# Performance work log

Hardware: AMD Instinct MI355X
Metric: run time of the kernel (lower is better)

## Reference

```python
import jax, jax.numpy as jnp
import numpy as np

B, S, D = 1, 4096, 768
H = 12
HD = D // H  # 64


def setup_inputs() -> dict:
    key = jax.random.key(0)
    ks = jax.random.split(key, 6)
    sc = 1.0 / np.sqrt(D)
    return {
        "x": jax.random.normal(ks[0], (B, S, D), dtype=jnp.float32),
        "wq": jax.random.normal(ks[1], (D, D), dtype=jnp.float32) * sc,
        "wk": jax.random.normal(ks[2], (D, D), dtype=jnp.float32) * sc,
        "wv": jax.random.normal(ks[3], (D, D), dtype=jnp.float32) * sc,
        "wo": jax.random.normal(ks[4], (D, D), dtype=jnp.float32) * sc,
        "bo": jax.random.normal(ks[5], (D,), dtype=jnp.float32) * 0.02,
    }


def reference(x, wq, wk, wv, wo, bo):
    b, n, _ = x.shape
    # projections (torch Linear: x @ W.T; here weights stored as (d_in, d_out))
    q = (x @ wq).reshape(b, n, H, HD).transpose(0, 2, 1, 3)  # b h n d
    k = (x @ wk).reshape(b, n, H, HD).transpose(0, 2, 1, 3)
    v = (x @ wv).reshape(b, n, H, HD).transpose(0, 2, 1, 3)
    scores = jnp.einsum("bhqd,bhkd->bhqk", q, k)
    causal = jnp.tril(jnp.ones((n, n), dtype=bool))  # True = keep
    scores = jnp.where(causal, scores, -jnp.inf)
    weights = jax.nn.softmax(scores / np.sqrt(HD), axis=-1)
    ctx = jnp.einsum("bhqk,bhkd->bhqd", weights, v)
    ctx = ctx.transpose(0, 2, 1, 3).reshape(b, n, D)
    return ctx @ wo + bo
```

## Files before the change

kernel.cpp:

```cpp
#include <hip/hip_runtime.h>


typedef short bf16x8 __attribute__((ext_vector_type(8)));
typedef float f32x4 __attribute__((ext_vector_type(4)));
typedef unsigned short u16;

static constexpr int S_LEN = 4096;
static constexpr int DIM   = 768;
static constexpr int NH    = 12;
static constexpr float QSCALE = 0.125f * 1.44269504088896340736f;

__device__ inline u16 f2bf(float f) {
  union { float f; unsigned int u; } v; v.f = f;
  unsigned int r = v.u + 0x7FFFu + ((v.u >> 16) & 1u);
  return (u16)(r >> 16);
}

__device__ inline void gload_lds16(const u16* g, u16* s) {
  __builtin_amdgcn_global_load_lds(
      (const __attribute__((address_space(1))) unsigned int*)g,
      (__attribute__((address_space(3))) unsigned int*)s, 16, 0, 0);
}

__global__ __launch_bounds__(256)
void prep_kernel(const float* __restrict__ x, const float* __restrict__ w0,
                 const float* __restrict__ w1, const float* __restrict__ w2,
                 const float* __restrict__ w3, u16* __restrict__ xb,
                 u16* __restrict__ t0, u16* __restrict__ t1,
                 u16* __restrict__ t2, u16* __restrict__ t3) {
  if (blockIdx.z == 4) {
    const size_t n = (size_t)S_LEN * DIM;
    const int id = blockIdx.y * 12 + blockIdx.x;
    const size_t stride = (size_t)144 * 256 * 8;
    for (size_t i = ((size_t)id * 256 + threadIdx.x) * 8; i < n; i += stride) {
      const float4 a = *(const float4*)(x + i);
      const float4 b = *(const float4*)(x + i + 4);
      bf16x8 o;
      o[0] = (short)f2bf(a.x); o[1] = (short)f2bf(a.y);
      o[2] = (short)f2bf(a.z); o[3] = (short)f2bf(a.w);
      o[4] = (short)f2bf(b.x); o[5] = (short)f2bf(b.y);
      o[6] = (short)f2bf(b.z); o[7] = (short)f2bf(b.w);
      *(bf16x8*)(xb + i) = o;
    }
    return;
  }
  __shared__ float T[64][65];
  const float* src; u16* dst;
  switch (blockIdx.z) {
    case 0: src = w0; dst = t0; break;
    case 1: src = w1; dst = t1; break;
    case 2: src = w2; dst = t2; break;
    default: src = w3; dst = t3; break;
  }
  const int k0 = blockIdx.y * 64, n0 = blockIdx.x * 64;
  const int r = threadIdx.x >> 2, c0 = (threadIdx.x & 3) * 16;
#pragma unroll
  for (int i = 0; i < 4; ++i) {
    const float4 v = *(const float4*)(src + (size_t)(k0 + r) * DIM + n0 + c0 + i * 4);
    T[r][c0 + i * 4 + 0] = v.x;
    T[r][c0 + i * 4 + 1] = v.y;
    T[r][c0 + i * 4 + 2] = v.z;
    T[r][c0 + i * 4 + 3] = v.w;
  }
  __syncthreads();
  bf16x8 o0, o1;
#pragma unroll
  for (int i = 0; i < 8; ++i) {
    o0[i] = (short)f2bf(T[c0 + i][r]);
    o1[i] = (short)f2bf(T[c0 + 8 + i][r]);
  }
  *(bf16x8*)(dst + (size_t)(n0 + r) * DIM + k0 + c0) = o0;
  *(bf16x8*)(dst + (size_t)(n0 + r) * DIM + k0 + c0 + 8) = o1;
}

template <int MODE>
__global__ __launch_bounds__(256)
void mfma_gemm_kernel(const u16* __restrict__ A, const u16* __restrict__ Bq,
                      const u16* __restrict__ Bk, const u16* __restrict__ Bv,
                      const float* __restrict__ bias, u16* __restrict__ Qb,
                      u16* __restrict__ Kb, u16* __restrict__ VT,
                      float* __restrict__ Out) {
  constexpr int MT = (MODE == 0) ? 4 : 2;
  constexpr int BM = MT * 32;
  __shared__ __align__(16) u16 Al[BM * 64];
  __shared__ __align__(16) u16 Bl[96 * 64];

  const int tid  = threadIdx.x;
  const int wv   = tid >> 6;
  const int lane = tid & 63;
  const int quad = lane >> 4;
  const int l16  = lane & 15;
  const int wr = wv >> 1, wc = wv & 1;
  const int m0 = blockIdx.y * BM;
  const int n0 = blockIdx.x * 96;

  int wi = 0, nb = n0;
  const u16* BT = Bq;
  if (MODE == 0) {
    wi = n0 / DIM;
    nb = n0 - wi * DIM;
    BT = (wi == 0) ? Bq : (wi == 1) ? Bk : Bv;
  }

  const int sr8 = lane >> 3;
  const int sc  = ((lane & 7) ^ sr8) * 8;
  const int key = (l16 & 7);

  f32x4 acc[MT][3] = {};

  for (int k0 = 0; k0 < DIM; k0 += 64) {
    __syncthreads();
#pragma unroll
    for (int j = 0; j < MT; ++j)
      gload_lds16(A + (size_t)(m0 + wv * (BM / 4) + j * 8 + sr8) * DIM + k0 + sc,
                  &Al[(wv * (BM / 4) + j * 8) * 64]);
#pragma unroll
    for (int j = 0; j < 3; ++j)
      gload_lds16(BT + (size_t)(nb + wv * 24 + j * 8 + sr8) * DIM + k0 + sc,
                  &Bl[(wv * 24 + j * 8) * 64]);
    __syncthreads();

#pragma unroll
    for (int kh = 0; kh < 2; ++kh) {
      const int cb = kh * 4;
      bf16x8 af[MT], bfr[3];
#pragma unroll
      for (int mt = 0; mt < MT; ++mt) {
        const int row = wr * (BM / 2) + mt * 16 + l16;
        af[mt] = *(const bf16x8*)&Al[row * 64 + ((cb + quad) ^ key) * 8];
      }
#pragma unroll
      for (int nt = 0; nt < 3; ++nt) {
        const int row = wc * 48 + nt * 16 + l16;
        bfr[nt] = *(const bf16x8*)&Bl[row * 64 + ((cb + quad) ^ key) * 8];
      }
#pragma unroll
      for (int mt = 0; mt < MT; ++mt)
#pragma unroll
        for (int nt = 0; nt < 3; ++nt)
          acc[mt][nt] = __builtin_amdgcn_mfma_f32_16x16x32_bf16(
              af[mt], bfr[nt], acc[mt][nt], 0, 0, 0);
    }
  }

  const float sc_out = (MODE == 0 && wi == 0) ? QSCALE : 1.0f;
#pragma unroll
  for (int mt = 0; mt < MT; ++mt) {
#pragma unroll
    for (int nt = 0; nt < 3; ++nt) {
      const int row = m0 + wr * (BM / 2) + mt * 16 + quad * 4;
      const int nc  = wc * 48 + nt * 16 + l16;
      if (MODE == 0) {
        const int ncol = nb + nc;
        if (wi < 2) {
          u16* dst = (wi == 0) ? Qb : Kb;
#pragma unroll
          for (int r = 0; r < 4; ++r)
            dst[(size_t)(row + r) * DIM + ncol] = f2bf(acc[mt][nt][r] * sc_out);
        } else {
          u16 pk[4];
#pragma unroll
          for (int r = 0; r < 4; ++r) pk[r] = f2bf(acc[mt][nt][r]);
          unsigned long long v;
          __builtin_memcpy(&v, pk, 8);
          *(unsigned long long*)(VT + (size_t)ncol * S_LEN + row) = v;
        }
      } else {
        const int ncol = n0 + nc;
        const float bvv = bias[ncol];
#pragma unroll
        for (int r = 0; r < 4; ++r)
          Out[(size_t)(row + r) * DIM + ncol] = acc[mt][nt][r] + bvv;
      }
    }
  }
}

__global__ __launch_bounds__(256)
void attn_mfma_kernel(const u16* __restrict__ Qb, const u16* __restrict__ Kb,
                      const u16* __restrict__ VTb, u16* __restrict__ ctx) {
  __shared__ __align__(16) u16 Ql[32 * 72];
  __shared__ __align__(16) u16 Kl[128 * 64];
  __shared__ __align__(16) u16 Vl[64 * 128];
  __shared__ __align__(16) u16 Pl[4][16 * 72];
  __shared__ float lbuf[256];

  const int tid  = threadIdx.x;
  const int w    = tid >> 6;
  const int lane = tid & 63;
  const int quad = lane >> 4;
  const int l16  = lane & 15;
  const int qw   = w >> 1;
  const int kw   = w & 1;
  const int key  = l16 & 7;

  const int id = blockIdx.x;
  const int rc = id & 7, slot = id >> 3;
  const int h  = (slot < 64) ? rc : 8 + (rc >> 1);
  const int bx = (slot < 64) ? slot : ((rc & 1) * 32 + (slot - 64));

  const int sr8  = lane >> 3;
  const int scK  = ((lane & 7) ^ sr8) * 8;
  const int sr16 = lane >> 4;

  bf16x8 ones;
#pragma unroll
  for (int i = 0; i < 8; ++i) ones[i] = (short)0x3F80;

#pragma unroll 1
  for (int side = 0; side < 2; ++side) {
    const int qt = side ? (127 - bx) : bx;
    const int q0 = qt * 32;

    __syncthreads();
    {
      const int row = tid >> 3, col = (tid & 7) * 8;
      *(bf16x8*)&Ql[row * 72 + col] =
          *(const bf16x8*)(Qb + (size_t)(q0 + row) * DIM + h * 64 + col);
    }

    f32x4 o[4] = {};
    f32x4 l_acc = {};

    const int nkt = qt / 2 + 1;
    const int niter = (nkt + 1) >> 1;
    const int my_last = nkt - 1;

#pragma unroll 1
    for (int i = 0; i < niter; ++i) {
      const int k0g = i * 128;
      __syncthreads();
#pragma unroll
      for (int j = 0; j < 4; ++j)
        gload_lds16(Kb + (size_t)(k0g + w * 32 + j * 8 + sr8) * DIM + h * 64 + scK,
                    &Kl[(w * 32 + j * 8) * 64]);
#pragma unroll
      for (int j = 0; j < 4; ++j) {
        const int vrow = w * 16 + j * 4 + sr16;
        const int vcol = ((lane & 15) ^ (vrow & 7)) * 8;
        gload_lds16(VTb + (size_t)(h * 64 + vrow) * S_LEN + k0g + vcol,
                    &Vl[(w * 16 + j * 4) * 128]);
      }
      __syncthreads();

      const int kt_w = 2 * i + kw;
      if (kt_w < nkt) {
        const bf16x8 aq0 = *(const bf16x8*)&Ql[(qw * 16 + l16) * 72 + quad * 8];
        const bf16x8 aq1 = *(const bf16x8*)&Ql[(qw * 16 + l16) * 72 + 32 + quad * 8];
        f32x4 s[4];
#pragma unroll
        for (int t = 0; t < 4; ++t) {
          const int row = kw * 64 + t * 16 + l16;
          const bf16x8 bk0 = *(const bf16x8*)&Kl[row * 64 + (quad ^ key) * 8];
          const bf16x8 bk1 = *(const bf16x8*)&Kl[row * 64 + ((quad ^ 4) ^ key) * 8];
          s[t] = __builtin_amdgcn_mfma_f32_16x16x32_bf16(aq0, bk0, f32x4{0.f,0.f,0.f,0.f}, 0, 0, 0);
          s[t] = __builtin_amdgcn_mfma_f32_16x16x32_bf16(aq1, bk1, s[t], 0, 0, 0);
        }

        if (kt_w == my_last) {
#pragma unroll
          for (int t = 0; t < 4; ++t)
#pragma unroll
            for (int r = 0; r < 4; ++r) {
              const int kvg = k0g + kw * 64 + t * 16 + l16;
              const int qg  = q0 + qw * 16 + quad * 4 + r;
              float p = __builtin_amdgcn_exp2f(s[t][r]);
              if (kvg > qg) p = 0.f;
              Pl[w][(quad * 4 + r) * 72 + t * 16 + l16] =
                  (u16)((__float_as_uint(p) + 0x8000u) >> 16);
            }
        } else {
#pragma unroll
          for (int t = 0; t < 4; ++t)
#pragma unroll
            for (int r = 0; r < 4; ++r) {
              const float p = __builtin_amdgcn_exp2f(s[t][r]);
              Pl[w][(quad * 4 + r) * 72 + t * 16 + l16] =
                  (u16)((__float_as_uint(p) + 0x8000u) >> 16);
            }
        }

        const bf16x8 pa0 = *(const bf16x8*)&Pl[w][l16 * 72 + quad * 8];
        const bf16x8 pa1 = *(const bf16x8*)&Pl[w][l16 * 72 + 32 + quad * 8];
#pragma unroll
        for (int t = 0; t < 4; ++t) {
          const int row = t * 16 + l16;
          const int c0 = (kw * 8 + quad) ^ key;
          const int c1 = (kw * 8 + quad + 4) ^ key;
          const bf16x8 vb0 = *(const bf16x8*)&Vl[row * 128 + c0 * 8];
          const bf16x8 vb1 = *(const bf16x8*)&Vl[row * 128 + c1 * 8];
          o[t] = __builtin_amdgcn_mfma_f32_16x16x32_bf16(vb0, pa0, o[t], 0, 0, 0);
          o[t] = __builtin_amdgcn_mfma_f32_16x16x32_bf16(vb1, pa1, o[t], 0, 0, 0);
        }
        l_acc = __builtin_amdgcn_mfma_f32_16x16x32_bf16(ones, pa0, l_acc, 0, 0, 0);
        l_acc = __builtin_amdgcn_mfma_f32_16x16x32_bf16(ones, pa1, l_acc, 0, 0, 0);
      }
    }

    __syncthreads();
    f32x4* Obuf = (f32x4*)Kl;
    const int ga = (kw == 0) ? 2 : 0;
    const int keep = 2 - ga;
    Obuf[(w * 2 + 0) * 64 + lane] = o[ga + 0];
    Obuf[(w * 2 + 1) * 64 + lane] = o[ga + 1];
    lbuf[w * 64 + lane] = l_acc[0];
    __syncthreads();
    o[keep + 0] += Obuf[((w ^ 1) * 2 + 0) * 64 + lane];
    o[keep + 1] += Obuf[((w ^ 1) * 2 + 1) * 64 + lane];
    const float l = l_acc[0] + lbuf[(w ^ 1) * 64 + lane];
    const float inv = 1.f / l;

    const int qrow = q0 + qw * 16 + l16;
#pragma unroll
    for (int s = 0; s < 2; ++s) {
      const int t = keep + s;
      u16 pk[4];
#pragma unroll
      for (int r = 0; r < 4; ++r) pk[r] = f2bf(o[t][r] * inv);
      unsigned long long v;
      __builtin_memcpy(&v, pk, 8);
      *(unsigned long long*)(ctx + (size_t)qrow * DIM + h * 64 + t * 16 + quad * 4) = v;
    }
  }
}

extern "C" void kernel_launch(void* const* d_in, const int* in_sizes, int n_in,
                              void* d_out, int out_size, void* d_ws,
                              size_t ws_size, hipStream_t stream) {
  const float* x  = (const float*)d_in[0];
  const float* wq = (const float*)d_in[1];
  const float* wk = (const float*)d_in[2];
  const float* wv = (const float*)d_in[3];
  const float* wo = (const float*)d_in[4];
  const float* bo = (const float*)d_in[5];

  const size_t n_x = (size_t)S_LEN * DIM;
  const size_t n_w = (size_t)DIM * DIM;
  u16* xb  = (u16*)d_ws;
  u16* wtq = xb + n_x;
  u16* wtk = wtq + n_w;
  u16* wtv = wtk + n_w;
  u16* wto = wtv + n_w;
  u16* Qb  = wto + n_w;
  u16* Kb  = Qb + n_x;
  u16* VTb = Kb + n_x;
  u16* ctx = VTb + n_x;

  prep_kernel<<<dim3(12, 12, 5), 256, 0, stream>>>(
      x, wq, wk, wv, wo, xb, wtq, wtk, wtv, wto);

  mfma_gemm_kernel<0><<<dim3(24, 32), 256, 0, stream>>>(
      xb, wtq, wtk, wtv, nullptr, Qb, Kb, VTb, nullptr);

  attn_mfma_kernel<<<dim3(768), 256, 0, stream>>>(Qb, Kb, VTb, ctx);

  mfma_gemm_kernel<1><<<dim3(8, 64), 256, 0, stream>>>(
      ctx, wto, nullptr, nullptr, bo, nullptr, nullptr, nullptr, (float*)d_out);
}
```

Baseline: 191.3 us.

## Load K/V/Q fragments directly from global memory instead of staging through LDS

The attention kernel stops staging Q, K and V^T tiles in shared memory with global_load_lds and block-wide barriers. Each wave now loads its own MFMA operand fragments straight from global memory into registers and walks its key tiles independently. The per-iteration __syncthreads are gone and LDS usage shrinks, which may allow higher occupancy. The cost is that the two query waves sharing a key tile now each fetch it separately, so the loads are redundant and less coalesced, and the extra register pressure and exposed global latency may outweigh the removed barriers.

After: 300.0 us. 56.9% more time.

```diff
diff --git a/kernel.cpp b/kernel.cpp
--- a/kernel.cpp
+++ b/kernel.cpp
@@ -179,11 +179,9 @@
 __global__ __launch_bounds__(256)
 void attn_mfma_kernel(const u16* __restrict__ Qb, const u16* __restrict__ Kb,
                       const u16* __restrict__ VTb, u16* __restrict__ ctx) {
-  __shared__ __align__(16) u16 Ql[32 * 72];
-  __shared__ __align__(16) u16 Kl[128 * 64];
-  __shared__ __align__(16) u16 Vl[64 * 128];
   __shared__ __align__(16) u16 Pl[4][16 * 72];
-  __shared__ float lbuf[256];
+  __shared__ __align__(16) f32x4 Obuf[8][64];
+  __shared__ float lbuf[4][64];
 
   const int tid  = threadIdx.x;
   const int w    = tid >> 6;
@@ -192,17 +190,12 @@
   const int l16  = lane & 15;
   const int qw   = w >> 1;
   const int kw   = w & 1;
-  const int key  = l16 & 7;
 
   const int id = blockIdx.x;
   const int rc = id & 7, slot = id >> 3;
   const int h  = (slot < 64) ? rc : 8 + (rc >> 1);
   const int bx = (slot < 64) ? slot : ((rc & 1) * 32 + (slot - 64));
 
-  const int sr8  = lane >> 3;
-  const int scK  = ((lane & 7) ^ sr8) * 8;
-  const int sr16 = lane >> 4;
-
   bf16x8 ones;
 #pragma unroll
   for (int i = 0; i < 8; ++i) ones[i] = (short)0x3F80;
@@ -212,102 +205,81 @@
     const int qt = side ? (127 - bx) : bx;
     const int q0 = qt * 32;
 
-    __syncthreads();
-    {
-      const int row = tid >> 3, col = (tid & 7) * 8;
-      *(bf16x8*)&Ql[row * 72 + col] =
-          *(const bf16x8*)(Qb + (size_t)(q0 + row) * DIM + h * 64 + col);
-    }
+    const u16* qptr = Qb + (size_t)(q0 + qw * 16 + l16) * DIM + h * 64 + quad * 8;
+    const bf16x8 aq0 = *(const bf16x8*)(qptr);
+    const bf16x8 aq1 = *(const bf16x8*)(qptr + 32);
 
     f32x4 o[4] = {};
     f32x4 l_acc = {};
 
     const int nkt = qt / 2 + 1;
-    const int niter = (nkt + 1) >> 1;
-    const int my_last = nkt - 1;
-
 #pragma unroll 1
-    for (int i = 0; i < niter; ++i) {
-      const int k0g = i * 128;
-      __syncthreads();
-#pragma unroll
-      for (int j = 0; j < 4; ++j)
-        gload_lds16(Kb + (size_t)(k0g + w * 32 + j * 8 + sr8) * DIM + h * 64 + scK,
-                    &Kl[(w * 32 + j * 8) * 64]);
-#pragma unroll
-      for (int j = 0; j < 4; ++j) {
-        const int vrow = w * 16 + j * 4 + sr16;
-        const int vcol = ((lane & 15) ^ (vrow & 7)) * 8;
-        gload_lds16(VTb + (size_t)(h * 64 + vrow) * S_LEN + k0g + vcol,
-                    &Vl[(w * 16 + j * 4) * 128]);
-      }
-      __syncthreads();
-
-      const int kt_w = 2 * i + kw;
-      if (kt_w < nkt) {
-        const bf16x8 aq0 = *(const bf16x8*)&Ql[(qw * 16 + l16) * 72 + quad * 8];
-        const bf16x8 aq1 = *(const bf16x8*)&Ql[(qw * 16 + l16) * 72 + 32 + quad * 8];
-        f32x4 s[4];
-#pragma unroll
-        for (int t = 0; t < 4; ++t) {
-          const int row = kw * 64 + t * 16 + l16;
-          const bf16x8 bk0 = *(const bf16x8*)&Kl[row * 64 + (quad ^ key) * 8];
-          const bf16x8 bk1 = *(const bf16x8*)&Kl[row * 64 + ((quad ^ 4) ^ key) * 8];
-          s[t] = __builtin_amdgcn_mfma_f32_16x16x32_bf16(aq0, bk0, f32x4{0.f,0.f,0.f,0.f}, 0, 0, 0);
-          s[t] = __builtin_amdgcn_mfma_f32_16x16x32_bf16(aq1, bk1, s[t], 0, 0, 0);
-        }
-
-        if (kt_w == my_last) {
-#pragma unroll
-          for (int t = 0; t < 4; ++t)
-#pragma unroll
-            for (int r = 0; r < 4; ++r) {
-              const int kvg = k0g + kw * 64 + t * 16 + l16;
-              const int qg  = q0 + qw * 16 + quad * 4 + r;
-              float p = __builtin_amdgcn_exp2f(s[t][r]);
-              if (kvg > qg) p = 0.f;
-              Pl[w][(quad * 4 + r) * 72 + t * 16 + l16] =
-                  (u16)((__float_as_uint(p) + 0x8000u) >> 16);
-            }
-        } else {
-#pragma unroll
-          for (int t = 0; t < 4; ++t)
-#pragma unroll
-            for (int r = 0; r < 4; ++r) {
-              const float p = __builtin_amdgcn_exp2f(s[t][r]);
-              Pl[w][(quad * 4 + r) * 72 + t * 16 + l16] =
-                  (u16)((__float_as_uint(p) + 0x8000u) >> 16);
-            }
-        }
-
-        const bf16x8 pa0 = *(const bf16x8*)&Pl[w][l16 * 72 + quad * 8];
-        const bf16x8 pa1 = *(const bf16x8*)&Pl[w][l16 * 72 + 32 + quad * 8];
-#pragma unroll
-        for (int t = 0; t < 4; ++t) {
-          const int row = t * 16 + l16;
-          const int c0 = (kw * 8 + quad) ^ key;
-          const int c1 = (kw * 8 + quad + 4) ^ key;
-          const bf16x8 vb0 = *(const bf16x8*)&Vl[row * 128 + c0 * 8];
-          const bf16x8 vb1 = *(const bf16x8*)&Vl[row * 128 + c1 * 8];
-          o[t] = __builtin_amdgcn_mfma_f32_16x16x32_bf16(vb0, pa0, o[t], 0, 0, 0);
-          o[t] = __builtin_amdgcn_mfma_f32_16x16x32_bf16(vb1, pa1, o[t], 0, 0, 0);
-        }
-        l_acc = __builtin_amdgcn_mfma_f32_16x16x32_bf16(ones, pa0, l_acc, 0, 0, 0);
-        l_acc = __builtin_amdgcn_mfma_f32_16x16x32_bf16(ones, pa1, l_acc, 0, 0, 0);
-      }
+    for (int kt = kw; kt < nkt; kt += 2) {
+      const int k0 = kt * 64;
+
+      const u16* kbase = Kb + (size_t)(k0 + l16) * DIM + h * 64 + quad * 8;
+      const u16* vbase = VTb + (size_t)(h * 64 + l16) * S_LEN + k0 + quad * 8;
+      bf16x8 bk0[4], bk1[4], vb0[4], vb1[4];
+#pragma unroll
+      for (int t = 0; t < 4; ++t) {
+        bk0[t] = *(const bf16x8*)(kbase + (size_t)t * 16 * DIM);
+        bk1[t] = *(const bf16x8*)(kbase + (size_t)t * 16 * DIM + 32);
+        vb0[t] = *(const bf16x8*)(vbase + (size_t)t * 16 * S_LEN);
+        vb1[t] = *(const bf16x8*)(vbase + (size_t)t * 16 * S_LEN + 32);
+      }
+
+      f32x4 s[4];
+#pragma unroll
+      for (int t = 0; t < 4; ++t) {
+        s[t] = __builtin_amdgcn_mfma_f32_16x16x32_bf16(
+            aq0, bk0[t], f32x4{0.f, 0.f, 0.f, 0.f}, 0, 0, 0);
+        s[t] = __builtin_amdgcn_mfma_f32_16x16x32_bf16(aq1, bk1[t], s[t], 0, 0, 0);
+      }
+
+      if (kt == nkt - 1) {
+#pragma unroll
+        for (int t = 0; t < 4; ++t)
+#pragma unroll
+          for (int r = 0; r < 4; ++r) {
+            const int kvg = k0 + t * 16 + l16;
+            const int qg  = q0 + qw * 16 + quad * 4 + r;
+            float p = __builtin_amdgcn_exp2f(s[t][r]);
+            if (kvg > qg) p = 0.f;
+            Pl[w][(quad * 4 + r) * 72 + t * 16 + l16] =
+                (u16)((__float_as_uint(p) + 0x8000u) >> 16);
+          }
+      } else {
+#pragma unroll
+        for (int t = 0; t < 4; ++t)
+#pragma unroll
+          for (int r = 0; r < 4; ++r) {
+            const float p = __builtin_amdgcn_exp2f(s[t][r]);
+            Pl[w][(quad * 4 + r) * 72 + t * 16 + l16] =
+                (u16)((__float_as_uint(p) + 0x8000u) >> 16);
+          }
+      }
+
+      const bf16x8 pa0 = *(const bf16x8*)&Pl[w][l16 * 72 + quad * 8];
+      const bf16x8 pa1 = *(const bf16x8*)&Pl[w][l16 * 72 + 32 + quad * 8];
+#pragma unroll
+      for (int t = 0; t < 4; ++t) {
+        o[t] = __builtin_amdgcn_mfma_f32_16x16x32_bf16(vb0[t], pa0, o[t], 0, 0, 0);
+        o[t] = __builtin_amdgcn_mfma_f32_16x16x32_bf16(vb1[t], pa1, o[t], 0, 0, 0);
+      }
+      l_acc = __builtin_amdgcn_mfma_f32_16x16x32_bf16(ones, pa0, l_acc, 0, 0, 0);
+      l_acc = __builtin_amdgcn_mfma_f32_16x16x32_bf16(ones, pa1, l_acc, 0, 0, 0);
     }
 
     __syncthreads();
-    f32x4* Obuf = (f32x4*)Kl;
     const int ga = (kw == 0) ? 2 : 0;
     const int keep = 2 - ga;
-    Obuf[(w * 2 + 0) * 64 + lane] = o[ga + 0];
-    Obuf[(w * 2 + 1) * 64 + lane] = o[ga + 1];
-    lbuf[w * 64 + lane] = l_acc[0];
+    Obuf[w * 2 + 0][lane] = o[ga + 0];
+    Obuf[w * 2 + 1][lane] = o[ga + 1];
+    lbuf[w][lane] = l_acc[0];
     __syncthreads();
-    o[keep + 0] += Obuf[((w ^ 1) * 2 + 0) * 64 + lane];
-    o[keep + 1] += Obuf[((w ^ 1) * 2 + 1) * 64 + lane];
-    const float l = l_acc[0] + lbuf[(w ^ 1) * 64 + lane];
+    o[keep + 0] += Obuf[(w ^ 1) * 2 + 0][lane];
+    o[keep + 1] += Obuf[(w ^ 1) * 2 + 1][lane];
+    const float l = l_acc[0] + lbuf[w ^ 1][lane];
     const float inv = 1.f / l;
 
     const int qrow = q0 + qw * 16 + l16;
```
